# Kernel tuning notes

Measured on AMD Instinct MI355X. Metric: run time of the kernel, lower is better.

## Reference

```python
import jax, jax.numpy as jnp
import numpy as np

D = 1024  # d_model (all ATTENTION_CONST widths)
N = 4096  # sequence length


def setup_inputs() -> dict:
    key = jax.random.key(0)
    ks = jax.random.split(key, 11)
    s = 1.0 / np.sqrt(D)
    return {
        "q": jax.random.normal(ks[0], (N, D), jnp.float32),
        "k": jax.random.normal(ks[1], (N, D), jnp.float32),
        "v": jax.random.normal(ks[2], (N, D), jnp.float32),
        "wq_w": jax.random.normal(ks[3], (D, D), jnp.float32) * s,
        "wq_b": jax.random.normal(ks[4], (D,), jnp.float32) * s,
        "wk_w": jax.random.normal(ks[5], (D, D), jnp.float32) * s,
        "wk_b": jax.random.normal(ks[6], (D,), jnp.float32) * s,
        "wv_w": jax.random.normal(ks[7], (D, D), jnp.float32) * s,
        "wv_b": jax.random.normal(ks[8], (D,), jnp.float32) * s,
        "wo_w": jax.random.normal(ks[9], (D, D), jnp.float32) * s,
        "wo_b": jax.random.normal(ks[10], (D,), jnp.float32) * s,
    }


def reference(q, k, v, wq_w, wq_b, wk_w, wk_b, wv_w, wv_b, wo_w, wo_b):
    # Linear projections (torch convention: y = x @ W.T + b)
    qp = q @ wq_w.T + wq_b  # [N, D]
    kp = k @ wk_w.T + wk_b  # [N, D]
    vp = v @ wv_w.T + wv_b  # [N, D]
    # Naive attention: NO sqrt(d) scaling, NO head split (faithful to source)
    scores = qp @ kp.T                      # [N, N]
    attention_weights = jax.nn.softmax(scores, axis=-1)
    x = attention_weights @ vp              # [N, D]
    x = x @ wo_w.T + wo_b                   # output projection
    return (x, attention_weights)
```

## Files before the change

kernel.cpp:

```cpp
#include <hip/hip_runtime.h>
#include <cstdint>

#define N_SEQ 4096
#define DMODEL 1024

#define BM 128
#define BN 128
#define BN2 64
#define UNITE 4096

typedef __bf16 bf16_t;
typedef _Float16 f16_t;
typedef f16_t f16x8 __attribute__((ext_vector_type(8)));
typedef f16_t f16x4 __attribute__((ext_vector_type(4)));
typedef float f32x4 __attribute__((ext_vector_type(4)));

typedef __attribute__((address_space(1))) void* as1ptr;
typedef __attribute__((address_space(3))) void* as3ptr;

__device__ __forceinline__ void gload16(const void* g, void* l) {
  __builtin_amdgcn_global_load_lds((as1ptr)(uintptr_t)g, (as3ptr)(uintptr_t)l,
                                   16, 0, 0);
}

__global__ __launch_bounds__(256)
void qkv_proj(const f16_t* __restrict__ qh, const f16_t* __restrict__ ql,
              const f16_t* __restrict__ wq, const float* __restrict__ wq_b,
              const f16_t* __restrict__ kh, const f16_t* __restrict__ kl,
              const f16_t* __restrict__ wk, const float* __restrict__ wk_b,
              const f16_t* __restrict__ vh, const f16_t* __restrict__ wv,
              const float* __restrict__ wv_b,
              f16_t* __restrict__ QPh, f16_t* __restrict__ QPl,
              f16_t* __restrict__ KPh, f16_t* __restrict__ VPt)
{
  __shared__ __align__(16) f16_t lds[6 * UNITE];

  const int z = blockIdx.z;
  const f16_t *A0, *A1 = nullptr, *B0;
  const float* bias;
  if (z == 0)      { A0 = qh; A1 = ql; B0 = wq; bias = wq_b; }
  else if (z == 1) { A0 = kh; A1 = kl; B0 = wk; bias = wk_b; }
  else             { A0 = vh;          B0 = wv; bias = wv_b; }
  const bool twop = (z < 2);

  const int M = N_SEQ, Nc = DMODEL, K = DMODEL;
  const int t = threadIdx.x;
  const int lane = t & 63;
  const int wave = t >> 6;
  const int wm = wave >> 1;
  const int wn = wave & 1;

  const int gx = gridDim.x;
  const int nwg = gx * gridDim.y;
  const int flat = blockIdx.y * gx + blockIdx.x;
  const int swz = (flat & 7) * (nwg >> 3) + (flat >> 3);
  const int row0 = (swz / gx) * BM;
  const int col0 = (swz % gx) * BN;

  const int srw = t >> 3;
  const int scol = 8 * ((t & 7) ^ ((t >> 3) & 7));
  const int sdst = t * 8;

  const int fr = lane & 15;
  const int kq = (lane >> 4) * 8;
  const int sw = (fr & 7) << 3;

  f32x4 acc[4][4] = {};

  for (int k0 = 0; k0 < K; k0 += 64) {
#pragma unroll
    for (int h = 0; h < 2; ++h) {
      const int r = h * 32 + srw;
      gload16(A0 + (size_t)(row0 + r) * K + k0 + scol,
              &lds[0 * UNITE + h * 2048 + sdst]);
      gload16(A0 + (size_t)(row0 + 64 + r) * K + k0 + scol,
              &lds[1 * UNITE + h * 2048 + sdst]);
      gload16(B0 + (size_t)(col0 + r) * K + k0 + scol,
              &lds[4 * UNITE + h * 2048 + sdst]);
      gload16(B0 + (size_t)(col0 + 64 + r) * K + k0 + scol,
              &lds[5 * UNITE + h * 2048 + sdst]);
      if (twop) {
        gload16(A1 + (size_t)(row0 + r) * K + k0 + scol,
                &lds[2 * UNITE + h * 2048 + sdst]);
        gload16(A1 + (size_t)(row0 + 64 + r) * K + k0 + scol,
                &lds[3 * UNITE + h * 2048 + sdst]);
      }
    }
    __syncthreads();

    f16x8 ah[4][2], al[4][2], bh[4][2];
#pragma unroll
    for (int m = 0; m < 4; ++m) {
      const int r = (m * 16 + fr) * 64;
#pragma unroll
      for (int ks = 0; ks < 2; ++ks) {
        const int c = (ks * 32 + kq) ^ sw;
        ah[m][ks] = *(const f16x8*)&lds[wm * UNITE + r + c];
        if (twop) al[m][ks] = *(const f16x8*)&lds[(2 + wm) * UNITE + r + c];
      }
    }
#pragma unroll
    for (int n = 0; n < 4; ++n) {
      const int r = (n * 16 + fr) * 64;
#pragma unroll
      for (int ks = 0; ks < 2; ++ks)
        bh[n][ks] = *(const f16x8*)&lds[(4 + wn) * UNITE + r +
                                        (((ks * 32 + kq)) ^ sw)];
    }

#pragma unroll
    for (int m = 0; m < 4; ++m)
#pragma unroll
      for (int n = 0; n < 4; ++n)
#pragma unroll
        for (int ks = 0; ks < 2; ++ks) {
          acc[m][n] = __builtin_amdgcn_mfma_f32_16x16x32_f16(
              ah[m][ks], bh[n][ks], acc[m][n], 0, 0, 0);
          if (twop)
            acc[m][n] = __builtin_amdgcn_mfma_f32_16x16x32_f16(
                al[m][ks], bh[n][ks], acc[m][n], 0, 0, 0);
        }
    __syncthreads();
  }

#pragma unroll
  for (int m = 0; m < 4; ++m) {
#pragma unroll
    for (int n = 0; n < 4; ++n) {
      const int grow0 = row0 + wm * 64 + m * 16 + (lane >> 4) * 4;
      const int gcol = col0 + wn * 64 + n * 16 + (lane & 15);
      const float bv = bias[gcol];
      if (z == 2) {
        f16x4 p;
#pragma unroll
        for (int r = 0; r < 4; ++r) p[r] = (f16_t)(acc[m][n][r] + bv);
        *(f16x4*)&VPt[(size_t)gcol * M + grow0] = p;
      } else if (z == 0) {
#pragma unroll
        for (int r = 0; r < 4; ++r) {
          const float val = acc[m][n][r] + bv;
          const size_t idx = (size_t)(grow0 + r) * Nc + gcol;
          const f16_t h = (f16_t)val;
          QPh[idx] = h;
          QPl[idx] = (f16_t)(val - (float)h);
        }
      } else {
#pragma unroll
        for (int r = 0; r < 4; ++r) {
          const float val = acc[m][n][r] + bv;
          KPh[(size_t)(grow0 + r) * Nc + gcol] = (f16_t)val;
        }
      }
    }
  }
}

template <int OUT_F32>
__global__ __launch_bounds__(256)
void gemm_f16e(const f16_t* __restrict__ A, const f16_t* __restrict__ B,
               const float* __restrict__ bias,
               f16_t* __restrict__ Cf16, float* __restrict__ Cf32,
               int M, int Nc, int K)
{
  __shared__ __align__(16) f16_t lds[6 * UNITE];

  const int gx = gridDim.x;
  const int nwg = gx * gridDim.y;
  const int flat = blockIdx.y * gx + blockIdx.x;
  const int swz = (flat & 7) * (nwg >> 3) + (flat >> 3);
  const int bx = swz % gx;
  const int by = swz / gx;

  const int t = threadIdx.x;
  const int lane = t & 63;
  const int wave = t >> 6;
  const int wm = wave >> 1;
  const int wn = wave & 1;
  const int row0 = by * BM;
  const int col0 = bx * BN2;

  const int srw = t >> 3;
  const int scol = 8 * ((t & 7) ^ ((t >> 3) & 7));
  const int sdst = t * 8;

  const int fr = lane & 15;
  const int kq = (lane >> 4) * 8;
  const int sw = (fr & 7) << 3;

  f32x4 acc[4][2] = {};

  for (int k0 = 0; k0 < K; k0 += 128) {
#pragma unroll
    for (int h = 0; h < 2; ++h) {
      const int r = h * 32 + srw;
      gload16(A + (size_t)(row0 + r) * K + k0 + scol,
              &lds[0 * UNITE + h * 2048 + sdst]);
      gload16(A + (size_t)(row0 + r) * K + k0 + 64 + scol,
              &lds[1 * UNITE + h * 2048 + sdst]);
      gload16(A + (size_t)(row0 + 64 + r) * K + k0 + scol,
              &lds[2 * UNITE + h * 2048 + sdst]);
      gload16(A + (size_t)(row0 + 64 + r) * K + k0 + 64 + scol,
              &lds[3 * UNITE + h * 2048 + sdst]);
      gload16(B + (size_t)(col0 + r) * K + k0 + scol,
              &lds[4 * UNITE + h * 2048 + sdst]);
      gload16(B + (size_t)(col0 + r) * K + k0 + 64 + scol,
              &lds[5 * UNITE + h * 2048 + sdst]);
    }
    __syncthreads();

    f16x8 ah[4][4], bh[2][4];
#pragma unroll
    for (int m = 0; m < 4; ++m) {
      const int r = (m * 16 + fr) * 64;
#pragma unroll
      for (int ks = 0; ks < 4; ++ks) {
        const int unit = wm * 2 + (ks >> 1);
        ah[m][ks] = *(const f16x8*)&lds[unit * UNITE + r +
                                        ((((ks & 1) * 32 + kq)) ^ sw)];
      }
    }
#pragma unroll
    for (int n = 0; n < 2; ++n) {
      const int r = (wn * 32 + n * 16 + fr) * 64;
#pragma unroll
      for (int ks = 0; ks < 4; ++ks) {
        const int unit = 4 + (ks >> 1);
        bh[n][ks] = *(const f16x8*)&lds[unit * UNITE + r +
                                        ((((ks & 1) * 32 + kq)) ^ sw)];
      }
    }

#pragma unroll
    for (int m = 0; m < 4; ++m)
#pragma unroll
      for (int n = 0; n < 2; ++n)
#pragma unroll
        for (int ks = 0; ks < 4; ++ks)
          acc[m][n] = __builtin_amdgcn_mfma_f32_16x16x32_f16(
              ah[m][ks], bh[n][ks], acc[m][n], 0, 0, 0);
    __syncthreads();
  }

#pragma unroll
  for (int m = 0; m < 4; ++m) {
#pragma unroll
    for (int n = 0; n < 2; ++n) {
      const int grow0 = row0 + wm * 64 + m * 16 + (lane >> 4) * 4;
      const int gcol = col0 + wn * 32 + n * 16 + (lane & 15);
#pragma unroll
      for (int r = 0; r < 4; ++r) {
        const size_t idx = (size_t)(grow0 + r) * Nc + gcol;
        if (OUT_F32) Cf32[idx] = acc[m][n][r] + bias[gcol];
        else         Cf16[idx] = (f16_t)acc[m][n][r];
      }
    }
  }
}

#define TILE_ELEMS 16384
#define UNIT_ELEMS 4096
#define NT_SC 32

template <int V> struct ic { static constexpr int value = V; };

#define SBAR() asm volatile("s_barrier" ::: "memory")
#define WAITLGKM(n)                                              \
  do {                                                           \
    asm volatile("s_waitcnt lgkmcnt(" #n ")" ::: "memory");      \
    __builtin_amdgcn_sched_barrier(0);                           \
  } while (0)

template <int MH>
__device__ __forceinline__ void load_A8f(const f16_t* Ab, int wm, int fr,
                                         int kq, int sw, f16x8 (&af)[4][2]) {
#pragma unroll
  for (int m = 0; m < 4; ++m) {
    const int row = wm * 128 + (MH * 4 + m) * 16 + fr;
#pragma unroll
    for (int ks = 0; ks < 2; ++ks)
      af[m][ks] = *(const f16x8*)&Ab[row * 64 + ((ks * 32 + kq) ^ sw)];
  }
}

template <int NH>
__device__ __forceinline__ void load_B4f(const f16_t* Bb, int wn, int fr,
                                         int kq, int sw, f16x8 (&bfr)[2][2]) {
#pragma unroll
  for (int n = 0; n < 2; ++n) {
    const int row = wn * 64 + (NH * 2 + n) * 16 + fr;
#pragma unroll
    for (int ks = 0; ks < 2; ++ks)
      bfr[n][ks] = *(const f16x8*)&Bb[row * 64 + ((ks * 32 + kq) ^ sw)];
  }
}

template <int MH, int NH>
__device__ __forceinline__ void mfma16f(const f16x8 (&af)[4][2],
                                        const f16x8 (&bfr)[2][2],
                                        f32x4 (&acc)[8][4]) {
#pragma unroll
  for (int m = 0; m < 4; ++m)
#pragma unroll
    for (int n = 0; n < 2; ++n)
#pragma unroll
      for (int ks = 0; ks < 2; ++ks)
        acc[MH * 4 + m][NH * 2 + n] = __builtin_amdgcn_mfma_f32_16x16x32_f16(
            af[m][ks], bfr[n][ks], acc[MH * 4 + m][NH * 2 + n], 0, 0, 0);
}

__global__ __launch_bounds__(512, 1)
void gemm8f_scores(const f16_t* __restrict__ Qh, const f16_t* __restrict__ Ql,
                   const f16_t* __restrict__ Kh, float* __restrict__ C)
{
  __shared__ __align__(16) f16_t sm[2 * 2 * TILE_ELEMS];

  const int t = threadIdx.x;
  const int lane = t & 63;
  const int wave = t >> 6;
  const int wm = wave >> 2;
  const int wn = wave & 3;

  const int flat = blockIdx.y * 16 + blockIdx.x;
  const int swzb = (flat & 7) * 32 + (flat >> 3);
  const int brow = (swzb >> 4) * 256;
  const int bcol = (swzb & 15) * 256;

  const int srow = t >> 3;
  const int scol = 8 * ((t & 7) ^ ((t >> 3) & 7));
  const int sdst = t * 8;

  const int fr = lane & 15;
  const int kq = (lane >> 4) * 8;
  const int sw = (fr & 7) << 3;

  auto stageA = [&](int buf, int u, int kt) {
    const f16_t* src = (kt >= 16) ? Ql : Qh;
    const int kk = (kt & 15) << 6;
    gload16(src + (size_t)(brow + u * 64 + srow) * DMODEL + kk + scol,
            &sm[(buf * 2 + 0) * TILE_ELEMS + u * UNIT_ELEMS + sdst]);
  };
  auto stageB = [&](int buf, int u, int kt) {
    const int kk = (kt & 15) << 6;
    gload16(Kh + (size_t)(bcol + u * 64 + srow) * DMODEL + kk + scol,
            &sm[(buf * 2 + 1) * TILE_ELEMS + u * UNIT_ELEMS + sdst]);
  };

  f32x4 acc[8][4] = {};
  f16x8 af0[4][2], af1[4][2];
  f16x8 b0[2][2], b1[2][2];

#pragma unroll
  for (int u = 0; u < 4; ++u) stageA(0, u, 0);
#pragma unroll
  for (int u = 0; u < 4; ++u) stageB(0, u, 0);
  stageA(1, 0, 1); stageA(1, 2, 1);
  stageB(1, 0, 1); stageB(1, 1, 1);
  stageA(1, 1, 1); stageA(1, 3, 1);
  asm volatile("s_waitcnt vmcnt(6)" ::: "memory");
  SBAR();

  auto tile = [&](auto Pc, int kt) {
    constexpr int p = decltype(Pc)::value;
    constexpr int q = p ^ 1;
    const bool n1 = (kt + 1 < NT_SC);
    const bool n2 = (kt + 2 < NT_SC);
    const f16_t* Ab = &sm[(p * 2 + 0) * TILE_ELEMS];
    const f16_t* Bb = &sm[(p * 2 + 1) * TILE_ELEMS];

    load_A8f<0>(Ab, wm, fr, kq, sw, af0);
    load_B4f<0>(Bb, wn, fr, kq, sw, b0);
    if (n1) { stageB(q, 2, kt + 1); stageB(q, 3, kt + 1); }
    load_B4f<1>(Bb, wn, fr, kq, sw, b1);
    WAITLGKM(4);
    __builtin_amdgcn_s_setprio(1);
    mfma16f<0, 0>(af0, b0, acc);
    __builtin_amdgcn_s_setprio(0);
    __builtin_amdgcn_sched_barrier(0);
    SBAR();

    if (n2) { stageA(p, 0, kt + 2); stageA(p, 2, kt + 2); }
    load_A8f<1>(Ab, wm, fr, kq, sw, af1);
    WAITLGKM(8);
    __builtin_amdgcn_s_setprio(1);
    mfma16f<0, 1>(af0, b1, acc);
    __builtin_amdgcn_s_setprio(0);
    __builtin_amdgcn_sched_barrier(0);
    SBAR();

    if (n2) { stageB(p, 0, kt + 2); stageB(p, 1, kt + 2); }
    WAITLGKM(0);
    __builtin_amdgcn_s_setprio(1);
    mfma16f<1, 0>(af1, b0, acc);
    __builtin_amdgcn_s_setprio(0);
    __builtin_amdgcn_sched_barrier(0);
    SBAR();

    if (n2) { stageA(p, 1, kt + 2); stageA(p, 3, kt + 2); }
    __builtin_amdgcn_s_setprio(1);
    mfma16f<1, 1>(af1, b1, acc);
    __builtin_amdgcn_s_setprio(0);
    __builtin_amdgcn_sched_barrier(0);
    if (n2)      asm volatile("s_waitcnt vmcnt(6)" ::: "memory");
    else if (n1) asm volatile("s_waitcnt vmcnt(0)" ::: "memory");
    SBAR();
  };

  for (int kt = 0; kt < NT_SC; kt += 2) {
    tile(ic<0>{}, kt);
    tile(ic<1>{}, kt + 1);
  }

#pragma unroll
  for (int mf = 0; mf < 8; ++mf) {
#pragma unroll
    for (int nf = 0; nf < 4; ++nf) {
      const int r0 = brow + wm * 128 + mf * 16 + (lane >> 4) * 4;
      const int c  = bcol + wn * 64 + nf * 16 + (lane & 15);
#pragma unroll
      for (int r = 0; r < 4; ++r)
        C[(size_t)(r0 + r) * N_SEQ + c] = acc[mf][nf][r];
    }
  }
}

struct SplitDesc {
  const float* src[7];
  f16_t* hi[7];
  f16_t* lo[7];
  int mode[7];
  int blk_start[8];
};

__global__ __launch_bounds__(256)
void split_all(SplitDesc d)
{
  const int b = blockIdx.x;
  int seg = 0;
#pragma unroll
  for (int s = 1; s < 7; ++s) seg += (b >= d.blk_start[s]) ? 1 : 0;
  const int i = (b - d.blk_start[seg]) * 256 + threadIdx.x;
  const float4 v = ((const float4*)d.src[seg])[i];
  const float vv[4] = {v.x, v.y, v.z, v.w};
  f16x4 h, l;
#pragma unroll
  for (int j = 0; j < 4; ++j) {
    const f16_t hh = (f16_t)vv[j];
    h[j] = hh;
    l[j] = (f16_t)(vv[j] - (float)hh);
  }
  ((f16x4*)d.hi[seg])[i] = h;
  if (d.mode[seg] == 2) ((f16x4*)d.lo[seg])[i] = l;
}

__global__ __launch_bounds__(256)
void softmax_rows(float* __restrict__ S, f16_t* __restrict__ P, int n)
{
  const int row = blockIdx.x;
  float* srow = S + (size_t)row * n;
  f16_t* prow = P + (size_t)row * n;
  const int t = threadIdx.x;
  const int lane = t & 63;
  const int wave = t >> 6;
  __shared__ float red[8];

  float4 v[4];
  float mx = -3.4e38f;
#pragma unroll
  for (int i = 0; i < 4; ++i) {
    v[i] = *(const float4*)(srow + (size_t)(i * 256 + t) * 4);
    mx = fmaxf(mx, fmaxf(fmaxf(v[i].x, v[i].y), fmaxf(v[i].z, v[i].w)));
  }
#pragma unroll
  for (int off = 32; off > 0; off >>= 1) mx = fmaxf(mx, __shfl_xor(mx, off));
  if (lane == 0) red[wave] = mx;
  __syncthreads();
  mx = fmaxf(fmaxf(red[0], red[1]), fmaxf(red[2], red[3]));

  float e[16];
  float sum = 0.f;
#pragma unroll
  for (int i = 0; i < 4; ++i) {
    e[4 * i + 0] = __expf(v[i].x - mx);
    e[4 * i + 1] = __expf(v[i].y - mx);
    e[4 * i + 2] = __expf(v[i].z - mx);
    e[4 * i + 3] = __expf(v[i].w - mx);
    sum += e[4 * i + 0] + e[4 * i + 1] + e[4 * i + 2] + e[4 * i + 3];
  }
#pragma unroll
  for (int off = 32; off > 0; off >>= 1) sum += __shfl_xor(sum, off);
  if (lane == 0) red[4 + wave] = sum;
  __syncthreads();
  sum = red[4] + red[5] + red[6] + red[7];
  const float inv = 1.0f / sum;

#pragma unroll
  for (int i = 0; i < 4; ++i) {
    float4 w;
    w.x = e[4 * i + 0] * inv;
    w.y = e[4 * i + 1] * inv;
    w.z = e[4 * i + 2] * inv;
    w.w = e[4 * i + 3] * inv;
    *(float4*)(srow + (size_t)(i * 256 + t) * 4) = w;
    f16x4 p;
    p[0] = (f16_t)w.x;
    p[1] = (f16_t)w.y;
    p[2] = (f16_t)w.z;
    p[3] = (f16_t)w.w;
    *(f16x4*)(prow + (size_t)(i * 256 + t) * 4) = p;
  }
}

extern "C" void kernel_launch(void* const* d_in, const int* in_sizes, int n_in,
                              void* d_out, int out_size, void* d_ws, size_t ws_size,
                              hipStream_t stream) {
  const int N = N_SEQ, D = DMODEL;
  const float* q    = (const float*)d_in[0];
  const float* k    = (const float*)d_in[1];
  const float* v    = (const float*)d_in[2];
  const float* wq_w = (const float*)d_in[3];
  const float* wq_b = (const float*)d_in[4];
  const float* wk_w = (const float*)d_in[5];
  const float* wk_b = (const float*)d_in[6];
  const float* wv_w = (const float*)d_in[7];
  const float* wv_b = (const float*)d_in[8];
  const float* wo_w = (const float*)d_in[9];
  const float* wo_b = (const float*)d_in[10];

  float* x_out = (float*)d_out;
  float* attn  = x_out + (size_t)N * D;

  char* wsp = (char*)d_ws;
  auto alloc = [&](size_t bytes) { char* p = wsp; wsp += bytes; return p; };
  const size_t ND = (size_t)N * D, DD = (size_t)D * D;
  f16_t*  qh16  = (f16_t*)alloc(ND * 2);
  f16_t*  ql16  = (f16_t*)alloc(ND * 2);
  f16_t*  kh16  = (f16_t*)alloc(ND * 2);
  f16_t*  kl16  = (f16_t*)alloc(ND * 2);
  f16_t*  vh16  = (f16_t*)alloc(ND * 2);
  f16_t*  wq16  = (f16_t*)alloc(DD * 2);
  f16_t*  wk16  = (f16_t*)alloc(DD * 2);
  f16_t*  wv16  = (f16_t*)alloc(DD * 2);
  f16_t*  wo16  = (f16_t*)alloc(DD * 2);
  f16_t*  QPh   = (f16_t*)alloc(ND * 2);
  f16_t*  QPl   = (f16_t*)alloc(ND * 2);
  f16_t*  KPh   = (f16_t*)alloc(ND * 2);
  f16_t*  spare = (f16_t*)alloc(ND * 2);
  f16_t*  VPt   = (f16_t*)alloc(ND * 2);
  f16_t*  Pb    = QPh;
  f16_t*  Xb    = vh16;
  (void)spare;

  SplitDesc sd;
  sd.src[0] = q;    sd.hi[0] = qh16;  sd.lo[0] = ql16;    sd.mode[0] = 2;
  sd.src[1] = k;    sd.hi[1] = kh16;  sd.lo[1] = kl16;    sd.mode[1] = 2;
  sd.src[2] = v;    sd.hi[2] = vh16;  sd.lo[2] = nullptr; sd.mode[2] = 3;
  sd.src[3] = wq_w; sd.hi[3] = wq16;  sd.lo[3] = nullptr; sd.mode[3] = 3;
  sd.src[4] = wk_w; sd.hi[4] = wk16;  sd.lo[4] = nullptr; sd.mode[4] = 3;
  sd.src[5] = wv_w; sd.hi[5] = wv16;  sd.lo[5] = nullptr; sd.mode[5] = 3;
  sd.src[6] = wo_w; sd.hi[6] = wo16;  sd.lo[6] = nullptr; sd.mode[6] = 3;
  const int nb_nd = (int)(ND / 4 / 256);
  const int nb_dd = (int)(DD / 4 / 256);
  sd.blk_start[0] = 0;
  sd.blk_start[1] = nb_nd;
  sd.blk_start[2] = 2 * nb_nd;
  sd.blk_start[3] = 3 * nb_nd;
  sd.blk_start[4] = 3 * nb_nd + nb_dd;
  sd.blk_start[5] = 3 * nb_nd + 2 * nb_dd;
  sd.blk_start[6] = 3 * nb_nd + 3 * nb_dd;
  sd.blk_start[7] = 3 * nb_nd + 4 * nb_dd;
  split_all<<<dim3(sd.blk_start[7]), dim3(256), 0, stream>>>(sd);

  const dim3 blk(256);
  const dim3 gsc(N / 256, N / 256);
  const dim3 gd(D / BN2, N / BM);

  qkv_proj<<<dim3(D / BN, N / BM, 3), blk, 0, stream>>>(
      qh16, ql16, wq16, wq_b,
      kh16, kl16, wk16, wk_b,
      vh16, wv16, wv_b,
      QPh, QPl, KPh, VPt);

  gemm8f_scores<<<gsc, dim3(512), 0, stream>>>(QPh, QPl, KPh, attn);

  softmax_rows<<<dim3(N), blk, 0, stream>>>(attn, Pb, N);

  gemm_f16e<0><<<gd, blk, 0, stream>>>(
      Pb, VPt, nullptr, Xb, nullptr, N, D, N);

  gemm_f16e<1><<<gd, blk, 0, stream>>>(
      Xb, wo16, wo_b, nullptr, x_out, N, D, D);
}
```

Measured before the change: 235.9 us.

## Double-buffer LDS in f16 GEMM with async prefetch of next K tiles

Rewrites the PV and output-projection GEMM kernel to use a two-stage LDS ping-pong with K-step 64 instead of a single 128-wide buffer with full syncthreads. Global-to-LDS loads for tile kt+2 are issued while computing tile kt, with explicit vmcnt/lgkmcnt waits and split MFMA batches so fragment loads overlap math. The aim is to hide global memory latency behind compute. The cost is more barriers per K step, since the step is halved, and tighter waitcnt bookkeeping.

```diff
diff --git a/kernel.cpp b/kernel.cpp
--- a/kernel.cpp
+++ b/kernel.cpp
@@ -22,6 +22,14 @@
   __builtin_amdgcn_global_load_lds((as1ptr)(uintptr_t)g, (as3ptr)(uintptr_t)l,
                                    16, 0, 0);
 }
+
+#define SBAR() asm volatile("s_barrier" ::: "memory")
+#define WAITLGKM(n)                                              \
+  do {                                                           \
+    asm volatile("s_waitcnt lgkmcnt(" #n ")" ::: "memory");      \
+    __builtin_amdgcn_sched_barrier(0);                           \
+  } while (0)
+#define WAITVM(n) asm volatile("s_waitcnt vmcnt(" #n ")" ::: "memory")
 
 __global__ __launch_bounds__(256)
 void qkv_proj(const f16_t* __restrict__ qh, const f16_t* __restrict__ ql,
@@ -157,12 +165,12 @@
 
 template <int OUT_F32>
 __global__ __launch_bounds__(256)
-void gemm_f16e(const f16_t* __restrict__ A, const f16_t* __restrict__ B,
+void gemm_f16p(const f16_t* __restrict__ A, const f16_t* __restrict__ B,
                const float* __restrict__ bias,
                f16_t* __restrict__ Cf16, float* __restrict__ Cf32,
                int M, int Nc, int K)
 {
-  __shared__ __align__(16) f16_t lds[6 * UNITE];
+  __shared__ __align__(16) f16_t lds[2 * 3 * UNITE];
 
   const int gx = gridDim.x;
   const int nwg = gx * gridDim.y;
@@ -187,58 +195,80 @@
   const int kq = (lane >> 4) * 8;
   const int sw = (fr & 7) << 3;
 
-  f32x4 acc[4][2] = {};
-
-  for (int k0 = 0; k0 < K; k0 += 128) {
+  auto stage = [&](int buf, int kt) {
+    const int k0 = kt << 6;
 #pragma unroll
     for (int h = 0; h < 2; ++h) {
       const int r = h * 32 + srw;
       gload16(A + (size_t)(row0 + r) * K + k0 + scol,
-              &lds[0 * UNITE + h * 2048 + sdst]);
-      gload16(A + (size_t)(row0 + r) * K + k0 + 64 + scol,
-              &lds[1 * UNITE + h * 2048 + sdst]);
+              &lds[(buf * 3 + 0) * UNITE + h * 2048 + sdst]);
       gload16(A + (size_t)(row0 + 64 + r) * K + k0 + scol,
-              &lds[2 * UNITE + h * 2048 + sdst]);
-      gload16(A + (size_t)(row0 + 64 + r) * K + k0 + 64 + scol,
-              &lds[3 * UNITE + h * 2048 + sdst]);
+              &lds[(buf * 3 + 1) * UNITE + h * 2048 + sdst]);
       gload16(B + (size_t)(col0 + r) * K + k0 + scol,
-              &lds[4 * UNITE + h * 2048 + sdst]);
-      gload16(B + (size_t)(col0 + r) * K + k0 + 64 + scol,
-              &lds[5 * UNITE + h * 2048 + sdst]);
-    }
-    __syncthreads();
-
-    f16x8 ah[4][4], bh[2][4];
-#pragma unroll
-    for (int m = 0; m < 4; ++m) {
-      const int r = (m * 16 + fr) * 64;
-#pragma unroll
-      for (int ks = 0; ks < 4; ++ks) {
-        const int unit = wm * 2 + (ks >> 1);
-        ah[m][ks] = *(const f16x8*)&lds[unit * UNITE + r +
-                                        ((((ks & 1) * 32 + kq)) ^ sw)];
-      }
-    }
-#pragma unroll
-    for (int n = 0; n < 2; ++n) {
-      const int r = (wn * 32 + n * 16 + fr) * 64;
-#pragma unroll
-      for (int ks = 0; ks < 4; ++ks) {
-        const int unit = 4 + (ks >> 1);
-        bh[n][ks] = *(const f16x8*)&lds[unit * UNITE + r +
-                                        ((((ks & 1) * 32 + kq)) ^ sw)];
-      }
-    }
-
-#pragma unroll
-    for (int m = 0; m < 4; ++m)
+              &lds[(buf * 3 + 2) * UNITE + h * 2048 + sdst]);
+    }
+  };
+
+  f32x4 acc[4][2] = {};
+  const int NT = K >> 6;
+
+  stage(0, 0);
+  stage(1, 1);
+  WAITVM(6);
+  SBAR();
+
+  for (int kt = 0; kt < NT; ++kt) {
+    const int p = kt & 1;
+    const f16_t* Ab = &lds[(p * 3 + wm) * UNITE];
+    const f16_t* Bb = &lds[(p * 3 + 2) * UNITE];
+
+    f16x8 ah[4][2], bh[2][2];
+#pragma unroll
+    for (int m = 0; m < 2; ++m)
+#pragma unroll
+      for (int ks = 0; ks < 2; ++ks)
+        ah[m][ks] = *(const f16x8*)&Ab[(m * 16 + fr) * 64 +
+                                       ((ks * 32 + kq) ^ sw)];
+#pragma unroll
+    for (int n = 0; n < 2; ++n)
+#pragma unroll
+      for (int ks = 0; ks < 2; ++ks)
+        bh[n][ks] = *(const f16x8*)&Bb[(wn * 32 + n * 16 + fr) * 64 +
+                                       ((ks * 32 + kq) ^ sw)];
+#pragma unroll
+    for (int m = 2; m < 4; ++m)
+#pragma unroll
+      for (int ks = 0; ks < 2; ++ks)
+        ah[m][ks] = *(const f16x8*)&Ab[(m * 16 + fr) * 64 +
+                                       ((ks * 32 + kq) ^ sw)];
+
+    WAITLGKM(4);
+#pragma unroll
+    for (int m = 0; m < 2; ++m)
 #pragma unroll
       for (int n = 0; n < 2; ++n)
 #pragma unroll
-        for (int ks = 0; ks < 4; ++ks)
+        for (int ks = 0; ks < 2; ++ks)
           acc[m][n] = __builtin_amdgcn_mfma_f32_16x16x32_f16(
               ah[m][ks], bh[n][ks], acc[m][n], 0, 0, 0);
-    __syncthreads();
+    WAITLGKM(0);
+#pragma unroll
+    for (int m = 2; m < 4; ++m)
+#pragma unroll
+      for (int n = 0; n < 2; ++n)
+#pragma unroll
+        for (int ks = 0; ks < 2; ++ks)
+          acc[m][n] = __builtin_amdgcn_mfma_f32_16x16x32_f16(
+              ah[m][ks], bh[n][ks], acc[m][n], 0, 0, 0);
+
+    SBAR();
+    if (kt + 2 < NT) {
+      stage(p, kt + 2);
+      WAITVM(6);
+    } else if (kt + 1 < NT) {
+      WAITVM(0);
+    }
+    SBAR();
   }
 
 #pragma unroll
@@ -262,13 +292,6 @@
 #define NT_SC 32
 
 template <int V> struct ic { static constexpr int value = V; };
-
-#define SBAR() asm volatile("s_barrier" ::: "memory")
-#define WAITLGKM(n)                                              \
-  do {                                                           \
-    asm volatile("s_waitcnt lgkmcnt(" #n ")" ::: "memory");      \
-    __builtin_amdgcn_sched_barrier(0);                           \
-  } while (0)
 
 template <int MH>
 __device__ __forceinline__ void load_A8f(const f16_t* Ab, int wm, int fr,
@@ -356,7 +379,7 @@
   stageA(1, 0, 1); stageA(1, 2, 1);
   stageB(1, 0, 1); stageB(1, 1, 1);
   stageA(1, 1, 1); stageA(1, 3, 1);
-  asm volatile("s_waitcnt vmcnt(6)" ::: "memory");
+  WAITVM(6);
   SBAR();
 
   auto tile = [&](auto Pc, int kt) {
@@ -400,8 +423,8 @@
     mfma16f<1, 1>(af1, b1, acc);
     __builtin_amdgcn_s_setprio(0);
     __builtin_amdgcn_sched_barrier(0);
-    if (n2)      asm volatile("s_waitcnt vmcnt(6)" ::: "memory");
-    else if (n1) asm volatile("s_waitcnt vmcnt(0)" ::: "memory");
+    if (n2)      WAITVM(6);
+    else if (n1) WAITVM(0);
     SBAR();
   };
 
@@ -584,9 +607,9 @@
 
   softmax_rows<<<dim3(N), blk, 0, stream>>>(attn, Pb, N);
 
-  gemm_f16e<0><<<gd, blk, 0, stream>>>(
+  gemm_f16p<0><<<gd, blk, 0, stream>>>(
       Pb, VPt, nullptr, Xb, nullptr, N, D, N);
 
-  gemm_f16e<1><<<gd, blk, 0, stream>>>(
+  gemm_f16p<1><<<gd, blk, 0, stream>>>(
       Xb, wo16, wo_b, nullptr, x_out, N, D, D);
 }
```

Result: faster. 219.4 us (-7.0%).
